# Kernel tuning notes

Hardware: AMD Instinct MI355X
Metric: run time of the kernel (lower is better)

The kernel has to match this reference:

```python
import jax, jax.numpy as jnp
import numpy as np

N, M, K = 100000, 50000, 32
G = 8            # GIBs per kind (cy, cone, disk, ellip)
OBS = 16         # num_observers
REACH = 1.0      # kernel_reach
EPS = 1e-8


def setup_inputs() -> dict:
    key = jax.random.key(0)
    ks = jax.random.split(key, 12)
    points = jax.random.normal(ks[0], (N, 3), dtype=jnp.float32)
    q_coords = jax.random.normal(ks[1], (M, 3), dtype=jnp.float32)
    support_idxs = jax.random.randint(ks[2], (M, K), 0, N)
    # per-GIB geometric parameters (random init, positive scales)
    cy_radius = jax.random.uniform(ks[3], (G,), minval=0.1, maxval=1.0)
    disk_radius = jax.random.uniform(ks[4], (G,), minval=0.1, maxval=1.0)
    disk_width = jax.random.uniform(ks[5], (G,), minval=0.05, maxval=0.5)
    cone_radius = jax.random.uniform(ks[6], (G,), minval=0.1, maxval=1.0)
    cone_inc = jax.random.uniform(ks[7], (G,), minval=0.0, maxval=1.0)
    ellip_radii = jax.random.uniform(ks[8], (G, 3), minval=0.1, maxval=1.0)
    # convex-combination coefficients: softmax over the GIB axis (maintain_convexity)
    lambdas = jax.nn.softmax(jax.random.normal(ks[9], (4 * G, OBS), dtype=jnp.float32), axis=0)
    return dict(points=points, q_coords=q_coords, support_idxs=support_idxs,
                cy_radius=cy_radius, disk_radius=disk_radius, disk_width=disk_width,
                cone_radius=cone_radius, cone_inc=cone_inc, ellip_radii=ellip_radii,
                lambdas=lambdas)


def _gib_outputs(points, q_coords, support_idxs, cy_radius, disk_radius,
                 disk_width, cone_radius, cone_inc, ellip_radii):
    # gather support points and form relative coordinates per query neighborhood
    rel = points[support_idxs] - q_coords[:, None, :]          # (M, K, 3)
    d2 = jnp.sum(rel * rel, axis=-1)                           # (M, K)
    mask = (d2 <= REACH * REACH).astype(rel.dtype)             # kernel reach mask
    xy2 = rel[..., 0] ** 2 + rel[..., 1] ** 2                  # (M, K)
    z = rel[..., 2]                                            # (M, K)

    def reduce(w):  # (M, K, G) -> (M, G): masked mean over support points
        return jnp.sum(w * mask[..., None], axis=1) / K

    # cylinder: gaussian of radial (xy) distance from the vertical axis
    w_cy = jnp.exp(-0.5 * xy2[..., None] / (cy_radius ** 2 + EPS))
    # cone: gaussian of distance to a cone surface of slope `inc`
    r_xy = jnp.sqrt(xy2 + EPS)
    w_cone = jnp.exp(-0.5 * (r_xy[..., None] - z[..., None] * cone_inc) ** 2
                     / (cone_radius ** 2 + EPS))
    # disk: gaussian in xy radius times gaussian in height
    w_disk = jnp.exp(-0.5 * (xy2[..., None] / (disk_radius ** 2 + EPS)
                             + (z[..., None] ** 2) / (disk_width ** 2 + EPS)))
    # ellipsoid: anisotropic gaussian with per-axis radii
    quad = jnp.einsum('mkd,gd->mkg', rel * rel, 1.0 / (ellip_radii ** 2 + EPS))
    w_ellip = jnp.exp(-0.5 * quad)

    return jnp.concatenate([reduce(w_cy), reduce(w_cone),
                            reduce(w_disk), reduce(w_ellip)], axis=-1)  # (M, 4G)


def reference(points, q_coords, support_idxs, cy_radius, disk_radius, disk_width,
              cone_radius, cone_inc, ellip_radii, lambdas):
    q_outputs = _gib_outputs(points, q_coords, support_idxs, cy_radius, disk_radius,
                             disk_width, cone_radius, cone_inc, ellip_radii)
    return q_outputs @ lambdas                                  # (M, OBS)
```

## Files before the change

kernel.cpp:

```cpp
#include <hip/hip_runtime.h>

#define KNBR 32
#define G 8
#define OBS 16
#define KP 4
#define TPQ 8
#define BLOCK 256

typedef float f4u __attribute__((ext_vector_type(4), aligned(4)));

__global__ __launch_bounds__(BLOCK, 6) void gib_kernel(
    const float* __restrict__ points,
    const float* __restrict__ q_coords,
    const int*   __restrict__ sidx,
    const float* __restrict__ cy_radius,
    const float* __restrict__ disk_radius,
    const float* __restrict__ disk_width,
    const float* __restrict__ cone_radius,
    const float* __restrict__ cone_inc,
    const float* __restrict__ ellip_radii,
    const float* __restrict__ lambdas,
    float* __restrict__ out,
    int M, int N)
{
    __shared__ __align__(16) float s_par[G * 8];
    __shared__ __align__(16) float s_lamT[OBS][36];
    __shared__ float4 s_feat[KP][BLOCK];
    __shared__ __align__(16) float s_acc[32][36];

    const float NL2E = -0.5f * 1.44269504088896340736f;
    const float EPS  = 1e-8f;

    const int t = threadIdx.x;
    if (t < G) {
        float r;
        r = cy_radius[t];        s_par[t*8 + 0] = NL2E / (r*r + EPS);
        s_par[t*8 + 1] = cone_inc[t];
        r = cone_radius[t];      s_par[t*8 + 2] = NL2E / (r*r + EPS);
        r = disk_radius[t];      s_par[t*8 + 3] = NL2E / (r*r + EPS);
        r = disk_width[t];       s_par[t*8 + 4] = NL2E / (r*r + EPS);
        float ra = ellip_radii[3*t+0];
        float rb = ellip_radii[3*t+1];
        float rc = ellip_radii[3*t+2];
        float ea = NL2E / (ra*ra + EPS);
        float eb = NL2E / (rb*rb + EPS);
        float ec = NL2E / (rc*rc + EPS);
        s_par[t*8 + 5] = eb;
        s_par[t*8 + 6] = ea - eb;
        s_par[t*8 + 7] = ec;
    }
    {
        int e0 = t, e1 = t + 256;
        s_lamT[e0 & 15][e0 >> 4] = lambdas[e0];
        s_lamT[e1 & 15][e1 >> 4] = lambdas[e1];
    }
    __syncthreads();

    const int gid = blockIdx.x * BLOCK + t;
    const int m   = gid >> 3;
    const int sub = t & 7;
    if (m >= M) return;

    const int4 iv = *(const int4*)(sidx + (size_t)m * KNBR + sub * KP);
    const int id[KP] = {iv.x, iv.y, iv.z, iv.w};

    const float qx = q_coords[3*m + 0];
    const float qy = q_coords[3*m + 1];
    const float qz = q_coords[3*m + 2];

    const int maxoff = 3 * N - 4;
    float px[KP], py[KP], pz[KP];
    #pragma unroll
    for (int j = 0; j < KP; j++) {
        int off  = 3 * id[j];
        int offc = off > maxoff ? maxoff : off;
        f4u p = *(const f4u*)(points + offc);
        bool sh = (off != offc);
        px[j] = sh ? p.y : p.x;
        py[j] = sh ? p.z : p.y;
        pz[j] = sh ? p.w : p.z;
    }

    unsigned am = 0;
    #pragma unroll
    for (int j = 0; j < KP; j++) {
        float rx = px[j]-qx, ry = py[j]-qy, rz = pz[j]-qz;
        float a = rx*rx, b = ry*ry, c = rz*rz;
        if (a + b + c <= 1.0f) am |= (1u << j);
        s_feat[j][t] = make_float4(a + b, a, c, rz);
    }
    am <<= (sub * 4);
    am |= __shfl_xor((int)am, 1);
    am |= __shfl_xor((int)am, 2);
    am |= __shfl_xor((int)am, 4);

    const float4 pA = *(const float4*)(s_par + sub*8);
    const float4 pB = *(const float4*)(s_par + sub*8 + 4);

    asm volatile("s_waitcnt lgkmcnt(0)" ::: "memory");

    float s0 = 0.f, s1 = 0.f, s2 = 0.f, s3 = 0.f;
    const int gbase = t & ~7;
    while (am) {
        const int slot = __builtin_ctz(am);
        am &= am - 1;
        float4 f = s_feat[slot & 3][gbase + (slot >> 2)];
        float xy2 = f.x, x2 = f.y, z2 = f.z, zz = f.w;
        float rxy = __builtin_amdgcn_sqrtf(xy2 + EPS);
        s0 += __builtin_amdgcn_exp2f(xy2 * pA.x);
        float d = __builtin_fmaf(-pA.y, zz, rxy);
        s1 += __builtin_amdgcn_exp2f(d * d * pA.z);
        s2 += __builtin_amdgcn_exp2f(__builtin_fmaf(xy2, pA.w, z2 * pB.x));
        s3 += __builtin_amdgcn_exp2f(__builtin_fmaf(xy2, pB.y,
                     __builtin_fmaf(x2, pB.z, z2 * pB.w)));
    }

    const int gq = t >> 3;
    float* arow = &s_acc[gq][sub];
    arow[0]  = s0;
    arow[8]  = s1;
    arow[16] = s2;
    arow[24] = s3;
    asm volatile("s_waitcnt lgkmcnt(0)" ::: "memory");

    const float4* av = (const float4*)s_acc[gq];
    const float4* l0 = (const float4*)s_lamT[2*sub];
    const float4* l1 = (const float4*)s_lamT[2*sub + 1];
    float o0 = 0.f, o1 = 0.f;
    #pragma unroll
    for (int r = 0; r < 8; r++) {
        float4 a4 = av[r], b0 = l0[r], b1 = l1[r];
        o0 = __builtin_fmaf(a4.x, b0.x, o0);
        o0 = __builtin_fmaf(a4.y, b0.y, o0);
        o0 = __builtin_fmaf(a4.z, b0.z, o0);
        o0 = __builtin_fmaf(a4.w, b0.w, o0);
        o1 = __builtin_fmaf(a4.x, b1.x, o1);
        o1 = __builtin_fmaf(a4.y, b1.y, o1);
        o1 = __builtin_fmaf(a4.z, b1.z, o1);
        o1 = __builtin_fmaf(a4.w, b1.w, o1);
    }

    const float s = 1.0f / (float)KNBR;
    *(float2*)(out + (size_t)m * OBS + sub*2) = make_float2(o0*s, o1*s);
}

extern "C" void kernel_launch(void* const* d_in, const int* in_sizes, int n_in,
                              void* d_out, int out_size, void* d_ws, size_t ws_size,
                              hipStream_t stream) {
    const float* points      = (const float*)d_in[0];
    const float* q_coords    = (const float*)d_in[1];
    const int*   sidx        = (const int*)  d_in[2];
    const float* cy_radius   = (const float*)d_in[3];
    const float* disk_radius = (const float*)d_in[4];
    const float* disk_width  = (const float*)d_in[5];
    const float* cone_radius = (const float*)d_in[6];
    const float* cone_inc    = (const float*)d_in[7];
    const float* ellip_radii = (const float*)d_in[8];
    const float* lambdas     = (const float*)d_in[9];
    float* out = (float*)d_out;

    const int N = in_sizes[0] / 3;
    const int M = in_sizes[1] / 3;
    const int grid = (M * TPQ + BLOCK - 1) / BLOCK;
    gib_kernel<<<grid, BLOCK, 0, stream>>>(points, q_coords, sidx,
                                           cy_radius, disk_radius, disk_width,
                                           cone_radius, cone_inc, ellip_radii,
                                           lambdas, out, M, N);
}
```

Before: 16.28 us.

## Use 16 threads per query with two GIB kinds each via unified coefficients

Each query is now handled by 16 threads, each gathering 2 neighbors instead of 4. Each thread evaluates 2 exponentials per masked neighbor instead of 4, using a per-lane coefficient table. That table merges cylinder/cone and disk/ellipsoid into one generic quadratic form per lane. Feature stores to LDS are skipped for out-of-reach neighbors, and the launch-bounds occupancy hint rises to 8. The aim is to spread the exp work and the gather latency over more threads, at the cost of more threads, one more shuffle round, and narrower loads and stores.

```diff
diff --git a/kernel.cpp b/kernel.cpp
--- a/kernel.cpp
+++ b/kernel.cpp
@@ -3,13 +3,13 @@
 #define KNBR 32
 #define G 8
 #define OBS 16
-#define KP 4
-#define TPQ 8
+#define KP 2
+#define TPQ 16
 #define BLOCK 256
 
 typedef float f4u __attribute__((ext_vector_type(4), aligned(4)));
 
-__global__ __launch_bounds__(BLOCK, 6) void gib_kernel(
+__global__ __launch_bounds__(BLOCK, 8) void gib_kernel(
     const float* __restrict__ points,
     const float* __restrict__ q_coords,
     const int*   __restrict__ sidx,
@@ -23,31 +23,45 @@
     float* __restrict__ out,
     int M, int N)
 {
-    __shared__ __align__(16) float s_par[G * 8];
+    __shared__ __align__(16) float s_kpar[16][8];
     __shared__ __align__(16) float s_lamT[OBS][36];
     __shared__ float4 s_feat[KP][BLOCK];
-    __shared__ __align__(16) float s_acc[32][36];
+    __shared__ __align__(16) float s_acc[BLOCK / TPQ][36];
 
     const float NL2E = -0.5f * 1.44269504088896340736f;
     const float EPS  = 1e-8f;
 
     const int t = threadIdx.x;
-    if (t < G) {
-        float r;
-        r = cy_radius[t];        s_par[t*8 + 0] = NL2E / (r*r + EPS);
-        s_par[t*8 + 1] = cone_inc[t];
-        r = cone_radius[t];      s_par[t*8 + 2] = NL2E / (r*r + EPS);
-        r = disk_radius[t];      s_par[t*8 + 3] = NL2E / (r*r + EPS);
-        r = disk_width[t];       s_par[t*8 + 4] = NL2E / (r*r + EPS);
-        float ra = ellip_radii[3*t+0];
-        float rb = ellip_radii[3*t+1];
-        float rc = ellip_radii[3*t+2];
-        float ea = NL2E / (ra*ra + EPS);
-        float eb = NL2E / (rb*rb + EPS);
-        float ec = NL2E / (rc*rc + EPS);
-        s_par[t*8 + 5] = eb;
-        s_par[t*8 + 6] = ea - eb;
-        s_par[t*8 + 7] = ec;
+    if (t < 16) {
+        const int g = t & 7;
+        float* kp = s_kpar[t];
+        if (t < 8) {
+            float r  = cy_radius[g];
+            float rc = cone_radius[g];
+            kp[0] = NL2E / (r * r + EPS);
+            kp[1] = 0.0f;
+            kp[2] = 1.0f;
+            kp[3] = -cone_inc[g];
+            kp[4] = NL2E / (rc * rc + EPS);
+            kp[5] = 0.0f; kp[6] = 0.0f; kp[7] = 0.0f;
+        } else {
+            float rd = disk_radius[g];
+            float rw = disk_width[g];
+            float ra = ellip_radii[3*g+0];
+            float rb = ellip_radii[3*g+1];
+            float rcc = ellip_radii[3*g+2];
+            float ea = NL2E / (ra * ra + EPS);
+            float eb = NL2E / (rb * rb + EPS);
+            float ec = NL2E / (rcc * rcc + EPS);
+            kp[0] = NL2E / (rd * rd + EPS);
+            kp[1] = NL2E / (rw * rw + EPS);
+            kp[2] = 0.0f;
+            kp[3] = 0.0f;
+            kp[4] = 0.0f;
+            kp[5] = eb;
+            kp[6] = ea - eb;
+            kp[7] = ec;
+        }
     }
     {
         int e0 = t, e1 = t + 256;
@@ -57,12 +71,12 @@
     __syncthreads();
 
     const int gid = blockIdx.x * BLOCK + t;
-    const int m   = gid >> 3;
-    const int sub = t & 7;
+    const int m   = gid >> 4;
+    const int sub = t & 15;
     if (m >= M) return;
 
-    const int4 iv = *(const int4*)(sidx + (size_t)m * KNBR + sub * KP);
-    const int id[KP] = {iv.x, iv.y, iv.z, iv.w};
+    const int2 iv = *(const int2*)(sidx + (size_t)m * KNBR + sub * KP);
+    const int id[KP] = {iv.x, iv.y};
 
     const float qx = q_coords[3*m + 0];
     const float qy = q_coords[3*m + 1];
@@ -86,62 +100,58 @@
     for (int j = 0; j < KP; j++) {
         float rx = px[j]-qx, ry = py[j]-qy, rz = pz[j]-qz;
         float a = rx*rx, b = ry*ry, c = rz*rz;
-        if (a + b + c <= 1.0f) am |= (1u << j);
-        s_feat[j][t] = make_float4(a + b, a, c, rz);
+        if (a + b + c <= 1.0f) {
+            am |= (1u << j);
+            s_feat[j][t] = make_float4(a + b, a, c, rz);
+        }
     }
-    am <<= (sub * 4);
+    am <<= (sub * 2);
     am |= __shfl_xor((int)am, 1);
     am |= __shfl_xor((int)am, 2);
     am |= __shfl_xor((int)am, 4);
+    am |= __shfl_xor((int)am, 8);
 
-    const float4 pA = *(const float4*)(s_par + sub*8);
-    const float4 pB = *(const float4*)(s_par + sub*8 + 4);
+    const float4 cA = *(const float4*)(s_kpar[sub]);
+    const float4 cB = *(const float4*)(s_kpar[sub] + 4);
 
     asm volatile("s_waitcnt lgkmcnt(0)" ::: "memory");
 
-    float s0 = 0.f, s1 = 0.f, s2 = 0.f, s3 = 0.f;
-    const int gbase = t & ~7;
+    float s0 = 0.f, s1 = 0.f;
+    const int gbase = t & ~15;
     while (am) {
         const int slot = __builtin_ctz(am);
         am &= am - 1;
-        float4 f = s_feat[slot & 3][gbase + (slot >> 2)];
-        float xy2 = f.x, x2 = f.y, z2 = f.z, zz = f.w;
-        float rxy = __builtin_amdgcn_sqrtf(xy2 + EPS);
-        s0 += __builtin_amdgcn_exp2f(xy2 * pA.x);
-        float d = __builtin_fmaf(-pA.y, zz, rxy);
-        s1 += __builtin_amdgcn_exp2f(d * d * pA.z);
-        s2 += __builtin_amdgcn_exp2f(__builtin_fmaf(xy2, pA.w, z2 * pB.x));
-        s3 += __builtin_amdgcn_exp2f(__builtin_fmaf(xy2, pB.y,
-                     __builtin_fmaf(x2, pB.z, z2 * pB.w)));
+        float4 f = s_feat[slot & 1][gbase + (slot >> 1)];
+        const float xy2 = f.x, x2 = f.y, z2 = f.z, zz = f.w;
+        const float rxy = __builtin_amdgcn_sqrtf(xy2 + EPS);
+        float q0 = __builtin_fmaf(xy2, cA.x, z2 * cA.y);
+        float d  = __builtin_fmaf(cA.z, rxy, cA.w * zz);
+        float q1 = __builtin_fmaf(d * d, cB.x,
+                     __builtin_fmaf(xy2, cB.y,
+                       __builtin_fmaf(x2, cB.z, z2 * cB.w)));
+        s0 += __builtin_amdgcn_exp2f(q0);
+        s1 += __builtin_amdgcn_exp2f(q1);
     }
 
-    const int gq = t >> 3;
-    float* arow = &s_acc[gq][sub];
-    arow[0]  = s0;
-    arow[8]  = s1;
-    arow[16] = s2;
-    arow[24] = s3;
+    const int gq = t >> 4;
+    float* arow = &s_acc[gq][(sub & 7) | ((sub & 8) << 1)];
+    arow[0] = s0;
+    arow[8] = s1;
     asm volatile("s_waitcnt lgkmcnt(0)" ::: "memory");
 
     const float4* av = (const float4*)s_acc[gq];
-    const float4* l0 = (const float4*)s_lamT[2*sub];
-    const float4* l1 = (const float4*)s_lamT[2*sub + 1];
-    float o0 = 0.f, o1 = 0.f;
+    const float4* lv = (const float4*)s_lamT[sub];
+    float o = 0.f;
     #pragma unroll
     for (int r = 0; r < 8; r++) {
-        float4 a4 = av[r], b0 = l0[r], b1 = l1[r];
-        o0 = __builtin_fmaf(a4.x, b0.x, o0);
-        o0 = __builtin_fmaf(a4.y, b0.y, o0);
-        o0 = __builtin_fmaf(a4.z, b0.z, o0);
-        o0 = __builtin_fmaf(a4.w, b0.w, o0);
-        o1 = __builtin_fmaf(a4.x, b1.x, o1);
-        o1 = __builtin_fmaf(a4.y, b1.y, o1);
-        o1 = __builtin_fmaf(a4.z, b1.z, o1);
-        o1 = __builtin_fmaf(a4.w, b1.w, o1);
+        float4 a4 = av[r], b4 = lv[r];
+        o = __builtin_fmaf(a4.x, b4.x, o);
+        o = __builtin_fmaf(a4.y, b4.y, o);
+        o = __builtin_fmaf(a4.z, b4.z, o);
+        o = __builtin_fmaf(a4.w, b4.w, o);
     }
 
-    const float s = 1.0f / (float)KNBR;
-    *(float2*)(out + (size_t)m * OBS + sub*2) = make_float2(o0*s, o1*s);
+    out[(size_t)m * OBS + sub] = o * (1.0f / (float)KNBR);
 }
 
 extern "C" void kernel_launch(void* const* d_in, const int* in_sizes, int n_in,
```

Result: no change. 16.00 us (-1.7%).
